# Kernel optimization log

Hardware: AMD Instinct MI355X
Metric: run time of the kernel (lower is better)

Reference implementation:

```python
import jax, jax.numpy as jnp
import numpy as np

GAMMA = 1.0        # soft-min temperature for differentiable DTW
BIG = 1e9          # value for cells outside the Sakoe-Chiba band
DTW_BW = 0.2       # band width as fraction of normalized path deviation
AVG_T_LEN = True   # divide discrepancy by input sequence length


def _softmin3(a, b, c):
    # differentiable min over the three DP predecessors
    z = jnp.stack([a, b, c], axis=0)
    return -GAMMA * jax.nn.logsumexp(-z / GAMMA, axis=0)


def _dtw(C, mask):
    """Band-limited soft-DTW DP. C: [T,K] pairwise costs, mask: [T,K] bool band.
    Returns scalar D[T-1,K-1]. Row scan over T; inner scan over K carries the
    left neighbor (recurrence D[i,j] = C[i,j] + softmin(D[i-1,j], D[i,j-1], D[i-1,j-1]))."""
    T, K = C.shape

    def row_step(carry, inp):
        prev_row, diag0 = carry            # prev_row: D[i-1,:]; diag0: virtual D[i-1,-1]
        c_row, m_row = inp
        diag = jnp.concatenate([diag0[None], prev_row[:-1]])  # D[i-1,j-1]

        def col_step(left, xs):
            c, up, dg, m = xs
            d = c + _softmin3(up, left, dg)
            d = jnp.where(m, d, BIG)       # kill cells outside the band
            return d, d

        _, row = jax.lax.scan(col_step, jnp.float32(BIG), (c_row, prev_row, diag, m_row))
        return (row, jnp.float32(BIG)), None

    # virtual border: D[-1,-1] = 0, all other border cells = BIG
    init = (jnp.full((K,), BIG, dtype=jnp.float32), jnp.float32(0.0))
    (last_row, _), _ = jax.lax.scan(row_step, init, (C, mask))
    return last_row[-1]


def setup_inputs() -> dict:
    key = jax.random.key(0)
    kx, kp = jax.random.split(key)
    B, T = 64, 512
    F, K = 32, 64
    x = jax.random.normal(kx, (B, T), dtype=jnp.float32)
    protos = jax.random.normal(kp, (F, K), dtype=jnp.float32)  # learnable DTW kernels
    return {"x": x, "protos": protos}


def reference(x, protos):
    B, T = x.shape
    F, K = protos.shape
    # pairwise squared costs: [B, F, T, K]
    C = (x[:, None, :, None] - protos[None, :, None, :]) ** 2
    # Sakoe-Chiba band on normalized coordinates
    ii = jnp.arange(T, dtype=jnp.float32) / (T - 1)
    jj = jnp.arange(K, dtype=jnp.float32) / (K - 1)
    mask = jnp.abs(ii[:, None] - jj[None, :]) <= DTW_BW  # [T, K]
    d = jax.vmap(jax.vmap(lambda c: _dtw(c, mask)))(C)    # [B, F]
    if AVG_T_LEN:
        d = d / jnp.float32(T)
    return d[:, :, None]  # [B, num_filter, out_len=1]
```

## Files before the change

kernel.cpp:

```cpp
#include <hip/hip_runtime.h>

#define T_LEN  512
#define K_LEN  64
#define NFILT  32
#define NBATCH 64
#define XOFS   64
#define XS_SZ  640
#define SQRT_LOG2E 1.2011224087864498f
#define LN2        0.6931471805599453f

static __device__ __forceinline__ float wave_shr1(float x) {
    int r = __builtin_amdgcn_update_dpp(0, __builtin_bit_cast(int, x),
                                        0x138, 0xF, 0xF, true);
    return __builtin_bit_cast(float, r);
}

template <int N>
static __device__ __forceinline__ float row_ror(float x) {
    int r = __builtin_amdgcn_update_dpp(0, __builtin_bit_cast(int, x),
                                        0x120 + N, 0xF, 0xF, true);
    return __builtin_bit_cast(float, r);
}

static __device__ __forceinline__ float exp2_fast(float x) {
#if __has_builtin(__builtin_amdgcn_exp2f)
    return __builtin_amdgcn_exp2f(x);
#else
    return exp2f(x);
#endif
}

__global__ __launch_bounds__(256) void dtw_kernel(const float* __restrict__ x,
                                                  const float* __restrict__ protos,
                                                  float* __restrict__ out) {
    __shared__ float xs[XS_SZ];
    const int tid  = threadIdx.x;
    const int lane = tid & 63;
    const int wid  = tid >> 6;
    const int b    = blockIdx.x >> 2;
    const int fA   = ((blockIdx.x & 3) << 2) | wid;
    const int fB   = fA + 16;

    for (int t0i = tid; t0i < XS_SZ; t0i += 256) {
        int i = t0i - XOFS;
        xs[t0i] = (i >= 0 && i < T_LEN) ? x[b * T_LEN + i] * SQRT_LOG2E : 0.0f;
    }
    __syncthreads();

    const float pAn = -protos[fA * K_LEN + lane] * SQRT_LOG2E;
    const float pBn = -protos[fB * K_LEN + lane] * SQRT_LOG2E;
    const float jj  = (float)lane / 63.0f;

    int a0 = 0, b0 = T_LEN - 1;
    while (a0 < b0) { int m = (a0 + b0) >> 1;
        if ((float)m / 511.0f - jj >= -0.2f) b0 = m; else a0 = m + 1; }
    const int ilo = a0;
    a0 = 0; b0 = T_LEN - 1;
    while (a0 < b0) { int m = (a0 + b0 + 1) >> 1;
        if ((float)m / 511.0f - jj <= 0.2f) a0 = m; else b0 = m - 1; }
    const int ihi = a0;

    const unsigned range = (unsigned)(ihi - ilo);
    unsigned t_chunk = (unsigned)(-(lane + ilo));
    float prevA = 0.0f, prevB = 0.0f;
    float dgpA  = (lane == 0) ? 1.0f : 0.0f;
    float dgpB  = dgpA;
    int   S2A = 0, S2B = 0;
    const float* bptr = &xs[XOFS - lane];

    float wA[32], wB[32];

#define BATCH32() do {                                                       \
        float xv_[32];                                                       \
        _Pragma("unroll")                                                    \
        for (int k = 0; k < 32; ++k) xv_[k] = bptr[k];                       \
        _Pragma("unroll")                                                    \
        for (int k = 0; k < 32; ++k) {                                       \
            unsigned tk_ = t_chunk + (unsigned)k;                            \
            float sel_ = (tk_ <= range) ? 0.0f : -3.0e38f;                   \
            float dA_ = xv_[k] + pAn;                                        \
            float dB_ = xv_[k] + pBn;                                        \
            wA[k] = exp2_fast(__builtin_fmaf(dA_, -dA_, sel_));              \
            wB[k] = exp2_fast(__builtin_fmaf(dB_, -dB_, sel_));              \
            asm volatile("" : "+v"(wA[k]), "+v"(wB[k]));                     \
        }                                                                    \
        t_chunk += 32; bptr += 32;                                           \
    } while (0)

#define CORE(N) do {                                                         \
        _Pragma("unroll")                                                    \
        for (int k = 0; k < (N); ++k) {                                      \
            float lA_ = wave_shr1(prevA);                                    \
            float lB_ = wave_shr1(prevB);                                    \
            float aA_ = prevA + dgpA;                                        \
            float aB_ = prevB + dgpB;                                        \
            dgpA = lA_; dgpB = lB_;                                          \
            prevA = (aA_ + lA_) * wA[k];                                     \
            prevB = (aB_ + lB_) * wB[k];                                     \
        }                                                                    \
    } while (0)

#define RENORM_HALF(PV, DG, S2) do {                                         \
        float m_ = PV;                                                       \
        m_ = fmaxf(m_, row_ror<8>(m_));                                      \
        m_ = fmaxf(m_, row_ror<4>(m_));                                      \
        m_ = fmaxf(m_, row_ror<2>(m_));                                      \
        m_ = fmaxf(m_, row_ror<1>(m_));                                      \
        int mi_ = __builtin_bit_cast(int, m_);                               \
        unsigned r0_ = (unsigned)__builtin_amdgcn_readlane(mi_, 0);          \
        unsigned r1_ = (unsigned)__builtin_amdgcn_readlane(mi_, 16);         \
        unsigned r2_ = (unsigned)__builtin_amdgcn_readlane(mi_, 32);         \
        unsigned r3_ = (unsigned)__builtin_amdgcn_readlane(mi_, 48);         \
        unsigned ra_ = r0_ > r1_ ? r0_ : r1_;                                \
        unsigned rb_ = r2_ > r3_ ? r2_ : r3_;                                \
        unsigned mx_ = ra_ > rb_ ? ra_ : rb_;                                \
        int e_  = (int)((mx_ >> 23) & 0xFF);                                 \
        int Me_ = 284 - e_;                                                  \
        Me_ = Me_ < 1 ? 1 : (Me_ > 254 ? 254 : Me_);                         \
        float M_ = __builtin_bit_cast(float, Me_ << 23);                     \
        S2 += Me_ - 127;                                                     \
        PV *= M_;                                                            \
        DG *= M_;                                                            \
    } while (0)

#define RENORM() do { RENORM_HALF(prevA, dgpA, S2A);                         \
                      RENORM_HALF(prevB, dgpB, S2B); } while (0)

#pragma unroll 1
    for (int c = 0; c < 17; ++c) {
        BATCH32();
        CORE(32);
        RENORM();
    }
    BATCH32();
    CORE(31);

    if (lane == 63) {
        float DA = ((float)S2A - log2f(prevA)) * LN2;
        float DB = ((float)S2B - log2f(prevB)) * LN2;
        out[b * NFILT + fA] = DA * (1.0f / (float)T_LEN);
        out[b * NFILT + fB] = DB * (1.0f / (float)T_LEN);
    }
#undef BATCH32
#undef CORE
#undef RENORM_HALF
#undef RENORM
}

extern "C" void kernel_launch(void* const* d_in, const int* in_sizes, int n_in,
                              void* d_out, int out_size, void* d_ws, size_t ws_size,
                              hipStream_t stream) {
    const float* x      = (const float*)d_in[0];
    const float* protos = (const float*)d_in[1];
    float* out          = (float*)d_out;

    dim3 grid(NBATCH * 4);
    dim3 block(256);
    hipLaunchKernelGGL(dtw_kernel, grid, block, 0, stream, x, protos, out);
}
```

Baseline: 28.46 us.

## Software-pipeline exp weight computation for next chunk with current DP wavefront steps

Restructures the chunked loop so the exp2 weights for the next 32-step chunk are computed in the same unrolled body as the current chunk's serial DPP recurrence. Register arrays are double-buffered and interleaved with sched_barrier, so independent transcendental work can hide the latency of the dependent shift/add/mul chain. This roughly doubles the weight register arrays and raises register pressure; launch_bounds(256,1) and a slightly larger shared buffer accommodate the extra prefetch.

```diff
diff --git a/kernel.cpp b/kernel.cpp
--- a/kernel.cpp
+++ b/kernel.cpp
@@ -5,7 +5,7 @@
 #define NFILT  32
 #define NBATCH 64
 #define XOFS   64
-#define XS_SZ  640
+#define XS_SZ  672
 #define SQRT_LOG2E 1.2011224087864498f
 #define LN2        0.6931471805599453f
 
@@ -30,9 +30,9 @@
 #endif
 }
 
-__global__ __launch_bounds__(256) void dtw_kernel(const float* __restrict__ x,
-                                                  const float* __restrict__ protos,
-                                                  float* __restrict__ out) {
+__global__ __launch_bounds__(256, 1) void dtw_kernel(const float* __restrict__ x,
+                                                     const float* __restrict__ protos,
+                                                     float* __restrict__ out) {
     __shared__ float xs[XS_SZ];
     const int tid  = threadIdx.x;
     const int lane = tid & 63;
@@ -61,44 +61,31 @@
     const int ihi = a0;
 
     const unsigned range = (unsigned)(ihi - ilo);
-    unsigned t_chunk = (unsigned)(-(lane + ilo));
+    unsigned tb = (unsigned)(-(lane + ilo));
     float prevA = 0.0f, prevB = 0.0f;
     float dgpA  = (lane == 0) ? 1.0f : 0.0f;
     float dgpB  = dgpA;
     int   S2A = 0, S2B = 0;
-    const float* bptr = &xs[XOFS - lane];
+    const float* bp = &xs[XOFS - lane];
 
-    float wA[32], wB[32];
+    float xvP[32], xvQ[32];
+    float wUA[32], wUB[32], wVA[32], wVB[32];
 
-#define BATCH32() do {                                                       \
-        float xv_[32];                                                       \
-        _Pragma("unroll")                                                    \
-        for (int k = 0; k < 32; ++k) xv_[k] = bptr[k];                       \
-        _Pragma("unroll")                                                    \
-        for (int k = 0; k < 32; ++k) {                                       \
-            unsigned tk_ = t_chunk + (unsigned)k;                            \
-            float sel_ = (tk_ <= range) ? 0.0f : -3.0e38f;                   \
-            float dA_ = xv_[k] + pAn;                                        \
-            float dB_ = xv_[k] + pBn;                                        \
-            wA[k] = exp2_fast(__builtin_fmaf(dA_, -dA_, sel_));              \
-            wB[k] = exp2_fast(__builtin_fmaf(dB_, -dB_, sel_));              \
-            asm volatile("" : "+v"(wA[k]), "+v"(wB[k]));                     \
-        }                                                                    \
-        t_chunk += 32; bptr += 32;                                           \
-    } while (0)
-
-#define CORE(N) do {                                                         \
-        _Pragma("unroll")                                                    \
-        for (int k = 0; k < (N); ++k) {                                      \
-            float lA_ = wave_shr1(prevA);                                    \
-            float lB_ = wave_shr1(prevB);                                    \
-            float aA_ = prevA + dgpA;                                        \
-            float aB_ = prevB + dgpB;                                        \
-            dgpA = lA_; dgpB = lB_;                                          \
-            prevA = (aA_ + lA_) * wA[k];                                     \
-            prevB = (aB_ + lB_) * wB[k];                                     \
-        }                                                                    \
-    } while (0)
+    {
+        float x0[32];
+#pragma unroll
+        for (int k = 0; k < 32; ++k) x0[k] = bp[k];
+#pragma unroll
+        for (int k = 0; k < 32; ++k) xvP[k] = bp[32 + k];
+#pragma unroll
+        for (int k = 0; k < 32; ++k) {
+            float sel = (tb <= range) ? 0.0f : -3.0e38f; ++tb;
+            float dA = x0[k] + pAn, dB = x0[k] + pBn;
+            wUA[k] = exp2_fast(__builtin_fmaf(dA, -dA, sel));
+            wUB[k] = exp2_fast(__builtin_fmaf(dB, -dB, sel));
+        }
+        bp += 64;
+    }
 
 #define RENORM_HALF(PV, DG, S2) do {                                         \
         float m_ = PV;                                                       \
@@ -126,14 +113,46 @@
 #define RENORM() do { RENORM_HALF(prevA, dgpA, S2A);                         \
                       RENORM_HALF(prevB, dgpB, S2B); } while (0)
 
+#define FUSED(XVU, XVF, WCA, WCB, WNA, WNB) do {                             \
+        _Pragma("unroll")                                                    \
+        for (int k = 0; k < 32; ++k) {                                       \
+            XVF[k] = bp[k + 0];          \
+            float sel_ = (tb <= range) ? 0.0f : -3.0e38f; ++tb;              \
+            float dA_ = XVU[k] + pAn;                                        \
+            float dB_ = XVU[k] + pBn;                                        \
+            WNA[k] = exp2_fast(__builtin_fmaf(dA_, -dA_, sel_));             \
+            WNB[k] = exp2_fast(__builtin_fmaf(dB_, -dB_, sel_));             \
+            asm volatile("" : "+v"(WNA[k]), "+v"(WNB[k]));                   \
+            float lA_ = wave_shr1(prevA);                                    \
+            float lB_ = wave_shr1(prevB);                                    \
+            float aA_ = prevA + dgpA;                                        \
+            float aB_ = prevB + dgpB;                                        \
+            dgpA = lA_; dgpB = lB_;                                          \
+            prevA = (aA_ + lA_) * WCA[k];                                    \
+            prevB = (aB_ + lB_) * WCB[k];                                    \
+            __builtin_amdgcn_sched_barrier(0);                               \
+        }                                                                    \
+        bp += 32;                                                            \
+        RENORM();                                                            \
+    } while (0)
+
 #pragma unroll 1
-    for (int c = 0; c < 17; ++c) {
-        BATCH32();
-        CORE(32);
-        RENORM();
+    for (int cc = 0; cc < 8; ++cc) {
+        FUSED(xvP, xvQ, wUA, wUB, wVA, wVB);
+        FUSED(xvQ, xvP, wVA, wVB, wUA, wUB);
     }
-    BATCH32();
-    CORE(31);
+    FUSED(xvP, xvQ, wUA, wUB, wVA, wVB);
+
+#pragma unroll
+    for (int k = 0; k < 31; ++k) {
+        float lA_ = wave_shr1(prevA);
+        float lB_ = wave_shr1(prevB);
+        float aA_ = prevA + dgpA;
+        float aB_ = prevB + dgpB;
+        dgpA = lA_; dgpB = lB_;
+        prevA = (aA_ + lA_) * wVA[k];
+        prevB = (aB_ + lB_) * wVB[k];
+    }
 
     if (lane == 63) {
         float DA = ((float)S2A - log2f(prevA)) * LN2;
@@ -141,8 +160,7 @@
         out[b * NFILT + fA] = DA * (1.0f / (float)T_LEN);
         out[b * NFILT + fB] = DB * (1.0f / (float)T_LEN);
     }
-#undef BATCH32
-#undef CORE
+#undef FUSED
 #undef RENORM_HALF
 #undef RENORM
 }
```

Result: slower. 30.64 us (+7.7%).
